# Kernel tuning notes

Hardware: AMD Instinct MI355X
Metric: run time of the kernel (lower is better)

## Reference

```python
import jax, jax.numpy as jnp
import numpy as np

HIDDEN = 1024
HEADS = 16
HEAD_DIM = HIDDEN // HEADS


def setup_inputs() -> dict:
    key = jax.random.key(0)
    ks = jax.random.split(key, 8)
    B, S = 2, 2048
    scale = 1.0 / np.sqrt(HIDDEN)
    inp = {
        "hidden_states": jax.random.normal(ks[0], (B, S, HIDDEN), dtype=jnp.float32),
        "attention_mask": jnp.zeros((B, 1, 1, S), dtype=jnp.float32),
        "q_w": jax.random.normal(ks[1], (HIDDEN, HIDDEN), dtype=jnp.float32) * scale,
        "q_b": jnp.zeros((HIDDEN,), dtype=jnp.float32),
        "k_w": jax.random.normal(ks[2], (HIDDEN, HIDDEN), dtype=jnp.float32) * scale,
        "k_b": jnp.zeros((HIDDEN,), dtype=jnp.float32),
        "v_w": jax.random.normal(ks[3], (HIDDEN, HIDDEN), dtype=jnp.float32) * scale,
        "v_b": jnp.zeros((HIDDEN,), dtype=jnp.float32),
    }
    return inp


def _split_heads(x):
    # [B, S, H] -> [B, heads, S, head_dim]
    B, S, _ = x.shape
    return x.reshape(B, S, HEADS, HEAD_DIM).transpose(0, 2, 1, 3)


def reference(hidden_states, attention_mask, q_w, q_b, k_w, k_b, v_w, v_b):
    # Linear projections (torch Linear: x @ W.T + b; here weights stored as [in, out])
    q = _split_heads(hidden_states @ q_w + q_b)  # [B, h, S, d]
    k = _split_heads(hidden_states @ k_w + k_b)
    v = _split_heads(hidden_states @ v_w + v_b)

    scores = jnp.einsum("bhqd,bhkd->bhqk", q, k) / jnp.sqrt(jnp.float32(HEAD_DIM))
    scores = scores + attention_mask  # additive mask, broadcast [B,1,1,S]
    probs = jax.nn.softmax(scores, axis=-1)
    # dropout prob = 0.0 -> identity
    ctx = jnp.einsum("bhqk,bhkd->bhqd", probs, v)  # [B, h, S, d]
    B, _, S, _ = ctx.shape
    ctx = ctx.transpose(0, 2, 1, 3).reshape(B, S, HIDDEN)
    return ctx
```

## Files before the change

kernel.cpp:

```cpp
#include <hip/hip_runtime.h>

typedef __bf16 bf16;
typedef __attribute__((ext_vector_type(8))) __bf16 bf16x8;
typedef __attribute__((ext_vector_type(4))) __bf16 bf16x4;
typedef __attribute__((ext_vector_type(4))) float f32x4;
typedef __attribute__((ext_vector_type(2))) unsigned int uint2v;
typedef __attribute__((ext_vector_type(4))) unsigned int uint4v;

#define MFMA(a, b, c) __builtin_amdgcn_mfma_f32_16x16x32_bf16((a), (b), (c), 0, 0, 0)
#define LOG2E 1.44269504088896340736f

__device__ __forceinline__ bf16x8 cvt8(float4 a, float4 b) {
  bf16x8 r;
  r[0] = (bf16)a.x; r[1] = (bf16)a.y; r[2] = (bf16)a.z; r[3] = (bf16)a.w;
  r[4] = (bf16)b.x; r[5] = (bf16)b.y; r[6] = (bf16)b.z; r[7] = (bf16)b.w;
  return r;
}

__device__ __forceinline__ void stage16(const bf16* g, bf16* l) {
  __builtin_amdgcn_global_load_lds(
      (const __attribute__((address_space(1))) void*)g,
      (__attribute__((address_space(3))) void*)l, 16, 0, 0);
}

__global__ __launch_bounds__(256)
void cvt(const float* __restrict__ hs, const float* __restrict__ qw,
         const float* __restrict__ kw, const float* __restrict__ vw,
         bf16* __restrict__ Xb, bf16* __restrict__ Wt) {
  const int bid = blockIdx.x, tid = threadIdx.x;
  if (bid < 2048) {
    size_t off = (size_t)bid * 2048 + tid * 8;
    float4 x0 = *(const float4*)(hs + off);
    float4 x1 = *(const float4*)(hs + off + 4);
    *(bf16x8*)(Xb + off) = cvt8(x0, x1);
  } else {
    int t = bid - 2048;
    int z = t >> 8, ti = t & 255;
    const float* W = (z == 0) ? qw : (z == 1) ? kw : vw;
    int k0 = (ti >> 4) * 64, n0 = (ti & 15) * 64;
    __shared__ bf16 T[64 * 72];
    #pragma unroll
    for (int i = 0; i < 16; ++i) {
      int e = i * 256 + tid;
      int kr = e >> 6, nc = e & 63;
      T[nc * 72 + kr] = (bf16)W[(size_t)(k0 + kr) * 1024 + n0 + nc];
    }
    __syncthreads();
    #pragma unroll
    for (int i = 0; i < 2; ++i) {
      int e = i * 256 + tid;
      int nr = e >> 3, kg = e & 7;
      *(bf16x8*)(Wt + (size_t)z * 1048576 + (size_t)(n0 + nr) * 1024 + k0 + kg * 8) =
          *(const bf16x8*)&T[nr * 72 + kg * 8];
    }
  }
}

__global__ __launch_bounds__(256, 3)
void qkv_gemm(const bf16* __restrict__ Xb, const bf16* __restrict__ Wt,
              const float* __restrict__ qbias, const float* __restrict__ kbias,
              const float* __restrict__ vbias,
              bf16* __restrict__ qo, bf16* __restrict__ ko, bf16* __restrict__ vo) {
  const int blk = blockIdx.x;
  const int xcd = blk & 7, slot = blk >> 3;
  const int mb = xcd * 4 + slot / 24;
  const int nb = slot % 24;
  const int z = nb >> 3, nbm = nb & 7;
  const bf16* W = Wt + (size_t)z * 1048576;

  const int tid = threadIdx.x;
  const int wave = tid >> 6, lane = tid & 63, quad = lane >> 4, c = lane & 15;
  const int wr = wave >> 1, wc = wave & 1;
  const int lrow = lane >> 3;
  const int lg = (lane & 7) ^ lrow;

  __shared__ bf16 As[128 * 64];
  __shared__ bf16 Bs[128 * 64];

  f32x4 acc[4][4] = {};

  for (int k0 = 0; k0 < 1024; k0 += 64) {
    #pragma unroll
    for (int i = 0; i < 4; ++i) {
      int r = wave * 32 + i * 8;
      stage16(Xb + (size_t)(mb * 128 + r + lrow) * 1024 + k0 + lg * 8, &As[r * 64]);
      stage16(W + (size_t)(nbm * 128 + r + lrow) * 1024 + k0 + lg * 8, &Bs[r * 64]);
    }
    __syncthreads();
    #pragma unroll
    for (int ch = 0; ch < 2; ++ch) {
      bf16x8 af[4];
      #pragma unroll
      for (int rt = 0; rt < 4; ++rt) {
        int row = wr * 64 + rt * 16 + c;
        af[rt] = *(const bf16x8*)&As[row * 64 + ((((ch << 2) | quad) ^ (c & 7)) << 3)];
      }
      #pragma unroll
      for (int nt = 0; nt < 4; ++nt) {
        int row = wc * 64 + nt * 16 + c;
        bf16x8 bfrag = *(const bf16x8*)&Bs[row * 64 + ((((ch << 2) | quad) ^ (c & 7)) << 3)];
        #pragma unroll
        for (int rt = 0; rt < 4; ++rt)
          acc[rt][nt] = MFMA(af[rt], bfrag, acc[rt][nt]);
      }
    }
    __syncthreads();
  }

  const float* bias = (z == 0) ? qbias : (z == 1) ? kbias : vbias;
  float bv[4];
  #pragma unroll
  for (int nt = 0; nt < 4; ++nt)
    bv[nt] = bias[nbm * 128 + wc * 64 + nt * 16 + c];

  if (z == 2) {
    #pragma unroll
    for (int rt = 0; rt < 4; ++rt)
      #pragma unroll
      for (int nt = 0; nt < 4; ++nt) {
        int m0 = mb * 128 + wr * 64 + rt * 16 + 4 * quad;
        int n = nbm * 128 + wc * 64 + nt * 16 + c;
        bf16x4 pk;
        #pragma unroll
        for (int reg = 0; reg < 4; ++reg) pk[reg] = (bf16)(acc[rt][nt][reg] + bv[nt]);
        int b = m0 >> 11, s0 = m0 & 2047, h = n >> 6, d = n & 63;
        *(bf16x4*)&vo[(((size_t)b * 16 + h) * 64 + d) * 2048 + s0] = pk;
      }
  } else {
    bf16* dst = (z == 0) ? qo : ko;
    const float scale = (z == 0) ? 0.125f * LOG2E : 1.0f;
    #pragma unroll
    for (int rt = 0; rt < 4; ++rt)
      #pragma unroll
      for (int nt = 0; nt < 4; ++nt)
        #pragma unroll
        for (int reg = 0; reg < 4; ++reg) {
          float v = (acc[rt][nt][reg] + bv[nt]) * scale;
          int m = mb * 128 + wr * 64 + rt * 16 + 4 * quad + reg;
          int n = nbm * 128 + wc * 64 + nt * 16 + c;
          int b = m >> 11, s = m & 2047, h = n >> 6, d = n & 63;
          dst[(((size_t)b * 16 + h) * 2048 + s) * 64 + d] = (bf16)v;
        }
  }
}

__global__ __launch_bounds__(256, 4)
void attn(const bf16* __restrict__ qg, const bf16* __restrict__ kg,
          const bf16* __restrict__ vtg, const float* __restrict__ mask,
          float* __restrict__ out) {
  const int blk = blockIdx.x;
  const int xcd = blk & 7, slot = blk >> 3;
  const int bh = xcd * 4 + (slot >> 4);
  const int qblk = slot & 15;
  const int b = bh >> 4, h = bh & 15;
  const int tid = threadIdx.x;
  const int wave = tid >> 6, lane = tid & 63, quad = lane >> 4, c = lane & 15;
  const int lrow = lane >> 3, lg = (lane & 7) ^ lrow;

  __shared__ __align__(16) bf16 Ks[2][64 * 64];
  __shared__ __align__(16) bf16 Vs[2][64 * 64];
  __shared__ __align__(16) float Ms[2048];

  const bf16* qb_ = qg + (size_t)bh * 2048 * 64;
  const bf16* kb_ = kg + (size_t)bh * 2048 * 64;
  const bf16* vb_ = vtg + (size_t)bh * 64 * 2048;

  #pragma unroll
  for (int i = 0; i < 2; ++i) {
    int idx = i * 1024 + tid * 4;
    float4 m = *(const float4*)&mask[b * 2048 + idx];
    float4 ms = {m.x * LOG2E, m.y * LOG2E, m.z * LOG2E, m.w * LOG2E};
    *(float4*)&Ms[idx] = ms;
  }

  bf16x8 qf[2][2];
  #pragma unroll
  for (int ct = 0; ct < 2; ++ct)
    #pragma unroll
    for (int ch = 0; ch < 2; ++ch)
      qf[ct][ch] = *(const bf16x8*)(qb_ +
          (size_t)(qblk * 128 + wave * 32 + ct * 16 + c) * 64 + ch * 32 + quad * 8);

  #pragma unroll
  for (int i = 0; i < 2; ++i) {
    int r = wave * 16 + i * 8;
    stage16(kb_ + (size_t)(r + lrow) * 64 + lg * 8, &Ks[0][r * 64]);
    stage16(vb_ + (size_t)(r + lrow) * 2048 + lg * 8, &Vs[0][r * 64]);
  }
  __asm__ volatile("s_waitcnt lgkmcnt(0)" ::: "memory");

  f32x4 o[2][4] = {};
  float lsum[2] = {0.f, 0.f};

  for (int kt = 0; kt < 32; ++kt) {
    const int cur = kt & 1;
    __asm__ volatile("s_waitcnt vmcnt(0)" ::: "memory");
    __builtin_amdgcn_s_barrier();
    __builtin_amdgcn_sched_barrier(0);

    if (kt < 31) {
      #pragma unroll
      for (int i = 0; i < 2; ++i) {
        int r = wave * 16 + i * 8;
        stage16(kb_ + (size_t)((kt + 1) * 64 + r + lrow) * 64 + lg * 8,
                &Ks[cur ^ 1][r * 64]);
        stage16(vb_ + (size_t)(r + lrow) * 2048 + (kt + 1) * 64 + lg * 8,
                &Vs[cur ^ 1][r * 64]);
      }
    }
    __builtin_amdgcn_sched_barrier(0);

    f32x4 s[2][4];
    #pragma unroll
    for (int nt = 0; nt < 4; ++nt) {
      float4 mv = *(const float4*)&Ms[kt * 64 + nt * 16 + 4 * quad];
      f32x4 sv = {mv.x, mv.y, mv.z, mv.w};
      s[0][nt] = sv;
      s[1][nt] = sv;
    }

    __builtin_amdgcn_s_setprio(1);
    #pragma unroll
    for (int nt = 0; nt < 4; ++nt)
      #pragma unroll
      for (int ch = 0; ch < 2; ++ch) {
        bf16x8 kf = *(const bf16x8*)&Ks[cur][(nt * 16 + c) * 64 +
                                            ((((ch << 2) | quad) ^ (c & 7)) << 3)];
        s[0][nt] = MFMA(kf, qf[0][ch], s[0][nt]);
        s[1][nt] = MFMA(kf, qf[1][ch], s[1][nt]);
      }
    __builtin_amdgcn_s_setprio(0);

    bf16x8 pa[2][2];
    #pragma unroll
    for (int ct = 0; ct < 2; ++ct) {
      unsigned int U[4][2];
      #pragma unroll
      for (int nt = 0; nt < 4; ++nt) {
        bf16x4 pk;
        #pragma unroll
        for (int reg = 0; reg < 4; ++reg) {
          float p = __builtin_amdgcn_exp2f(s[ct][nt][reg]);
          lsum[ct] += p;
          pk[reg] = (bf16)p;
        }
        uint2v uu = __builtin_bit_cast(uint2v, pk);
        U[nt][0] = uu.x; U[nt][1] = uu.y;
      }
      #pragma unroll
      for (int ch = 0; ch < 2; ++ch) {
        unsigned int X0 = U[2 * ch][0],     X1 = U[2 * ch][1];
        unsigned int Y0 = U[2 * ch + 1][0], Y1 = U[2 * ch + 1][1];
        __asm__ volatile("v_permlane32_swap_b32 %0, %1" : "+v"(X0), "+v"(Y0));
        __asm__ volatile("v_permlane32_swap_b32 %0, %1" : "+v"(X1), "+v"(Y1));
        __asm__ volatile("v_permlane16_swap_b32 %0, %1" : "+v"(X0), "+v"(Y0));
        __asm__ volatile("v_permlane16_swap_b32 %0, %1" : "+v"(X1), "+v"(Y1));
        uint4v up = {X0, X1, Y0, Y1};
        pa[ct][ch] = __builtin_bit_cast(bf16x8, up);
      }
    }

    __builtin_amdgcn_s_setprio(1);
    #pragma unroll
    for (int ch = 0; ch < 2; ++ch)
      #pragma unroll
      for (int nt = 0; nt < 4; ++nt) {
        bf16x8 vf = *(const bf16x8*)&Vs[cur][(nt * 16 + c) * 64 +
                                            ((((ch << 2) | quad) ^ (c & 7)) << 3)];
        o[0][nt] = MFMA(vf, pa[0][ch], o[0][nt]);
        o[1][nt] = MFMA(vf, pa[1][ch], o[1][nt]);
      }
    __builtin_amdgcn_s_setprio(0);
  }

  #pragma unroll
  for (int ct = 0; ct < 2; ++ct) {
    float l = lsum[ct];
    l += __shfl_xor(l, 16, 64);
    l += __shfl_xor(l, 32, 64);
    const float inv = 1.0f / l;
    const int srow = qblk * 128 + wave * 32 + ct * 16 + c;
    #pragma unroll
    for (int nt = 0; nt < 4; ++nt) {
      float4 st = { o[ct][nt][0] * inv, o[ct][nt][1] * inv,
                    o[ct][nt][2] * inv, o[ct][nt][3] * inv };
      *(float4*)&out[((size_t)b * 2048 + srow) * 1024 + h * 64 + nt * 16 + 4 * quad] = st;
    }
  }
}

extern "C" void kernel_launch(void* const* d_in, const int* in_sizes, int n_in,
                              void* d_out, int out_size, void* d_ws, size_t ws_size,
                              hipStream_t stream) {
  const float* hs   = (const float*)d_in[0];
  const float* mask = (const float*)d_in[1];
  const float* qw   = (const float*)d_in[2];
  const float* qb   = (const float*)d_in[3];
  const float* kw   = (const float*)d_in[4];
  const float* kb   = (const float*)d_in[5];
  const float* vw   = (const float*)d_in[6];
  const float* vb   = (const float*)d_in[7];
  float* out = (float*)d_out;

  bf16* Xb   = (bf16*)d_ws;
  bf16* Wt   = Xb + (size_t)4096 * 1024;
  bf16* q_ws = Wt + (size_t)3 * 1048576;
  bf16* k_ws = q_ws + (size_t)4096 * 1024;
  bf16* v_ws = k_ws + (size_t)4096 * 1024;

  cvt<<<dim3(2816), 256, 0, stream>>>(hs, qw, kw, vw, Xb, Wt);
  qkv_gemm<<<dim3(768), 256, 0, stream>>>(Xb, Wt, qb, kb, vb, q_ws, k_ws, v_ws);
  attn<<<dim3(512), 256, 0, stream>>>(q_ws, k_ws, v_ws, mask, out);
}
```

Before: 167.0 us.

## Stage V-transpose through LDS for coalesced stores; double attention key tile per barrier

In the QKV GEMM, the V output tile is now transposed through shared memory (padded row stride 136) and written as contiguous 16-byte chunks along the sequence dimension. Previously each lane did scattered 8-byte stores. In the attention kernel, each pipeline stage now loads two 64-key K/V tiles instead of one, which halves the number of barriers and waits per block. The cost is double the LDS per attention block, and occupancy is capped at 2 blocks per CU instead of 4.

```diff
diff --git a/kernel.cpp b/kernel.cpp
--- a/kernel.cpp
+++ b/kernel.cpp
@@ -74,8 +74,9 @@
   const int lrow = lane >> 3;
   const int lg = (lane & 7) ^ lrow;
 
-  __shared__ bf16 As[128 * 64];
-  __shared__ bf16 Bs[128 * 64];
+  __shared__ __align__(16) bf16 SH[128 * 136];
+  bf16* As = SH;
+  bf16* Bs = SH + 8192;
 
   f32x4 acc[4][4] = {};
 
@@ -118,14 +119,22 @@
     for (int rt = 0; rt < 4; ++rt)
       #pragma unroll
       for (int nt = 0; nt < 4; ++nt) {
-        int m0 = mb * 128 + wr * 64 + rt * 16 + 4 * quad;
-        int n = nbm * 128 + wc * 64 + nt * 16 + c;
         bf16x4 pk;
         #pragma unroll
         for (int reg = 0; reg < 4; ++reg) pk[reg] = (bf16)(acc[rt][nt][reg] + bv[nt]);
-        int b = m0 >> 11, s0 = m0 & 2047, h = n >> 6, d = n & 63;
-        *(bf16x4*)&vo[(((size_t)b * 16 + h) * 64 + d) * 2048 + s0] = pk;
-      }
+        int nl = wc * 64 + nt * 16 + c;
+        int sl = wr * 64 + rt * 16 + 4 * quad;
+        *(bf16x4*)&SH[nl * 136 + sl] = pk;
+      }
+    __syncthreads();
+    const int row = tid >> 1, sc = tid & 1;
+    const int hloc = row >> 6, d = row & 63;
+    const int bq = mb >> 4;
+    const int sg = (mb * 128) & 2047;
+    bf16* dst = vo + (((size_t)bq * 16 + nbm * 2 + hloc) * 64 + d) * 2048 + sg + sc * 64;
+    #pragma unroll
+    for (int j = 0; j < 8; ++j)
+      *(bf16x8*)&dst[j * 8] = *(const bf16x8*)&SH[row * 136 + sc * 64 + j * 8];
   } else {
     bf16* dst = (z == 0) ? qo : ko;
     const float scale = (z == 0) ? 0.125f * LOG2E : 1.0f;
@@ -144,7 +153,7 @@
   }
 }
 
-__global__ __launch_bounds__(256, 4)
+__global__ __launch_bounds__(256, 2)
 void attn(const bf16* __restrict__ qg, const bf16* __restrict__ kg,
           const bf16* __restrict__ vtg, const float* __restrict__ mask,
           float* __restrict__ out) {
@@ -157,8 +166,8 @@
   const int wave = tid >> 6, lane = tid & 63, quad = lane >> 4, c = lane & 15;
   const int lrow = lane >> 3, lg = (lane & 7) ^ lrow;
 
-  __shared__ __align__(16) bf16 Ks[2][64 * 64];
-  __shared__ __align__(16) bf16 Vs[2][64 * 64];
+  __shared__ __align__(16) bf16 Ks[2][2][64 * 64];
+  __shared__ __align__(16) bf16 Vs[2][2][64 * 64];
   __shared__ __align__(16) float Ms[2048];
 
   const bf16* qb_ = qg + (size_t)bh * 2048 * 64;
@@ -182,95 +191,102 @@
           (size_t)(qblk * 128 + wave * 32 + ct * 16 + c) * 64 + ch * 32 + quad * 8);
 
   #pragma unroll
-  for (int i = 0; i < 2; ++i) {
-    int r = wave * 16 + i * 8;
-    stage16(kb_ + (size_t)(r + lrow) * 64 + lg * 8, &Ks[0][r * 64]);
-    stage16(vb_ + (size_t)(r + lrow) * 2048 + lg * 8, &Vs[0][r * 64]);
-  }
+  for (int kh = 0; kh < 2; ++kh)
+    #pragma unroll
+    for (int i = 0; i < 2; ++i) {
+      int r = wave * 16 + i * 8;
+      stage16(kb_ + (size_t)(kh * 64 + r + lrow) * 64 + lg * 8, &Ks[0][kh][r * 64]);
+      stage16(vb_ + (size_t)(r + lrow) * 2048 + kh * 64 + lg * 8, &Vs[0][kh][r * 64]);
+    }
   __asm__ volatile("s_waitcnt lgkmcnt(0)" ::: "memory");
 
   f32x4 o[2][4] = {};
   float lsum[2] = {0.f, 0.f};
 
-  for (int kt = 0; kt < 32; ++kt) {
+  for (int kt = 0; kt < 16; ++kt) {
     const int cur = kt & 1;
     __asm__ volatile("s_waitcnt vmcnt(0)" ::: "memory");
     __builtin_amdgcn_s_barrier();
     __builtin_amdgcn_sched_barrier(0);
 
-    if (kt < 31) {
-      #pragma unroll
-      for (int i = 0; i < 2; ++i) {
-        int r = wave * 16 + i * 8;
-        stage16(kb_ + (size_t)((kt + 1) * 64 + r + lrow) * 64 + lg * 8,
-                &Ks[cur ^ 1][r * 64]);
-        stage16(vb_ + (size_t)(r + lrow) * 2048 + (kt + 1) * 64 + lg * 8,
-                &Vs[cur ^ 1][r * 64]);
-      }
+    if (kt < 15) {
+      #pragma unroll
+      for (int kh = 0; kh < 2; ++kh)
+        #pragma unroll
+        for (int i = 0; i < 2; ++i) {
+          int r = wave * 16 + i * 8;
+          stage16(kb_ + (size_t)((kt + 1) * 128 + kh * 64 + r + lrow) * 64 + lg * 8,
+                  &Ks[cur ^ 1][kh][r * 64]);
+          stage16(vb_ + (size_t)(r + lrow) * 2048 + (kt + 1) * 128 + kh * 64 + lg * 8,
+                  &Vs[cur ^ 1][kh][r * 64]);
+        }
     }
     __builtin_amdgcn_sched_barrier(0);
 
-    f32x4 s[2][4];
-    #pragma unroll
-    for (int nt = 0; nt < 4; ++nt) {
-      float4 mv = *(const float4*)&Ms[kt * 64 + nt * 16 + 4 * quad];
-      f32x4 sv = {mv.x, mv.y, mv.z, mv.w};
-      s[0][nt] = sv;
-      s[1][nt] = sv;
-    }
-
-    __builtin_amdgcn_s_setprio(1);
-    #pragma unroll
-    for (int nt = 0; nt < 4; ++nt)
-      #pragma unroll
-      for (int ch = 0; ch < 2; ++ch) {
-        bf16x8 kf = *(const bf16x8*)&Ks[cur][(nt * 16 + c) * 64 +
-                                            ((((ch << 2) | quad) ^ (c & 7)) << 3)];
-        s[0][nt] = MFMA(kf, qf[0][ch], s[0][nt]);
-        s[1][nt] = MFMA(kf, qf[1][ch], s[1][nt]);
-      }
-    __builtin_amdgcn_s_setprio(0);
-
-    bf16x8 pa[2][2];
-    #pragma unroll
-    for (int ct = 0; ct < 2; ++ct) {
-      unsigned int U[4][2];
+    #pragma unroll
+    for (int kh = 0; kh < 2; ++kh) {
+      f32x4 s[2][4];
       #pragma unroll
       for (int nt = 0; nt < 4; ++nt) {
-        bf16x4 pk;
-        #pragma unroll
-        for (int reg = 0; reg < 4; ++reg) {
-          float p = __builtin_amdgcn_exp2f(s[ct][nt][reg]);
-          lsum[ct] += p;
-          pk[reg] = (bf16)p;
-        }
-        uint2v uu = __builtin_bit_cast(uint2v, pk);
-        U[nt][0] = uu.x; U[nt][1] = uu.y;
-      }
-      #pragma unroll
-      for (int ch = 0; ch < 2; ++ch) {
-        unsigned int X0 = U[2 * ch][0],     X1 = U[2 * ch][1];
-        unsigned int Y0 = U[2 * ch + 1][0], Y1 = U[2 * ch + 1][1];
-        __asm__ volatile("v_permlane32_swap_b32 %0, %1" : "+v"(X0), "+v"(Y0));
-        __asm__ volatile("v_permlane32_swap_b32 %0, %1" : "+v"(X1), "+v"(Y1));
-        __asm__ volatile("v_permlane16_swap_b32 %0, %1" : "+v"(X0), "+v"(Y0));
-        __asm__ volatile("v_permlane16_swap_b32 %0, %1" : "+v"(X1), "+v"(Y1));
-        uint4v up = {X0, X1, Y0, Y1};
-        pa[ct][ch] = __builtin_bit_cast(bf16x8, up);
-      }
-    }
-
-    __builtin_amdgcn_s_setprio(1);
-    #pragma unroll
-    for (int ch = 0; ch < 2; ++ch)
-      #pragma unroll
-      for (int nt = 0; nt < 4; ++nt) {
-        bf16x8 vf = *(const bf16x8*)&Vs[cur][(nt * 16 + c) * 64 +
-                                            ((((ch << 2) | quad) ^ (c & 7)) << 3)];
-        o[0][nt] = MFMA(vf, pa[0][ch], o[0][nt]);
-        o[1][nt] = MFMA(vf, pa[1][ch], o[1][nt]);
-      }
-    __builtin_amdgcn_s_setprio(0);
+        float4 mv = *(const float4*)&Ms[kt * 128 + kh * 64 + nt * 16 + 4 * quad];
+        f32x4 sv = {mv.x, mv.y, mv.z, mv.w};
+        s[0][nt] = sv;
+        s[1][nt] = sv;
+      }
+
+      __builtin_amdgcn_s_setprio(1);
+      #pragma unroll
+      for (int nt = 0; nt < 4; ++nt)
+        #pragma unroll
+        for (int ch = 0; ch < 2; ++ch) {
+          bf16x8 kf = *(const bf16x8*)&Ks[cur][kh][(nt * 16 + c) * 64 +
+                                              ((((ch << 2) | quad) ^ (c & 7)) << 3)];
+          s[0][nt] = MFMA(kf, qf[0][ch], s[0][nt]);
+          s[1][nt] = MFMA(kf, qf[1][ch], s[1][nt]);
+        }
+      __builtin_amdgcn_s_setprio(0);
+
+      bf16x8 pa[2][2];
+      #pragma unroll
+      for (int ct = 0; ct < 2; ++ct) {
+        unsigned int U[4][2];
+        #pragma unroll
+        for (int nt = 0; nt < 4; ++nt) {
+          bf16x4 pk;
+          #pragma unroll
+          for (int reg = 0; reg < 4; ++reg) {
+            float p = __builtin_amdgcn_exp2f(s[ct][nt][reg]);
+            lsum[ct] += p;
+            pk[reg] = (bf16)p;
+          }
+          uint2v uu = __builtin_bit_cast(uint2v, pk);
+          U[nt][0] = uu.x; U[nt][1] = uu.y;
+        }
+        #pragma unroll
+        for (int ch = 0; ch < 2; ++ch) {
+          unsigned int X0 = U[2 * ch][0],     X1 = U[2 * ch][1];
+          unsigned int Y0 = U[2 * ch + 1][0], Y1 = U[2 * ch + 1][1];
+          __asm__ volatile("v_permlane32_swap_b32 %0, %1" : "+v"(X0), "+v"(Y0));
+          __asm__ volatile("v_permlane32_swap_b32 %0, %1" : "+v"(X1), "+v"(Y1));
+          __asm__ volatile("v_permlane16_swap_b32 %0, %1" : "+v"(X0), "+v"(Y0));
+          __asm__ volatile("v_permlane16_swap_b32 %0, %1" : "+v"(X1), "+v"(Y1));
+          uint4v up = {X0, X1, Y0, Y1};
+          pa[ct][ch] = __builtin_bit_cast(bf16x8, up);
+        }
+      }
+
+      __builtin_amdgcn_s_setprio(1);
+      #pragma unroll
+      for (int ch = 0; ch < 2; ++ch)
+        #pragma unroll
+        for (int nt = 0; nt < 4; ++nt) {
+          bf16x8 vf = *(const bf16x8*)&Vs[cur][kh][(nt * 16 + c) * 64 +
+                                              ((((ch << 2) | quad) ^ (c & 7)) << 3)];
+          o[0][nt] = MFMA(vf, pa[0][ch], o[0][nt]);
+          o[1][nt] = MFMA(vf, pa[1][ch], o[1][nt]);
+        }
+      __builtin_amdgcn_s_setprio(0);
+    }
   }
 
   #pragma unroll
```

After: 168.8 us. Within noise of the previous version (+1.1%).
